# Optimization experiments

Measured on AMD Instinct MI355X. Metric: run time of the kernel, lower is better.

The kernel has to match this reference:

```python
import jax, jax.numpy as jnp
import numpy as np

EPS = 1e-5


def setup_inputs() -> dict:
    key = jax.random.key(0)
    ks = jax.random.split(key, 12)
    B, C, D, H, W = 16, 32, 32, 64, 64
    HID, OUT = 256, 128
    inp = {
        "x": jax.random.normal(ks[0], (B, C, D, H, W), dtype=jnp.float32),
        "bn_gamma": jax.random.normal(ks[1], (C,), dtype=jnp.float32) * 0.1 + 1.0,
        "bn_beta": jax.random.normal(ks[2], (C,), dtype=jnp.float32) * 0.1,
        "w_ih": jax.random.normal(ks[3], (HID, C), dtype=jnp.float32) / np.sqrt(C),
        "b_ih": jax.random.normal(ks[4], (HID,), dtype=jnp.float32) * 0.01,
        "w_hh": jax.random.normal(ks[5], (HID, HID), dtype=jnp.float32) / np.sqrt(HID),
        "b_hh": jax.random.normal(ks[6], (HID,), dtype=jnp.float32) * 0.01,
        "w_out": jax.random.normal(ks[7], (OUT, HID), dtype=jnp.float32) / np.sqrt(HID),
        "b_out": jax.random.normal(ks[8], (OUT,), dtype=jnp.float32) * 0.01,
        "ln_gamma": jnp.ones((OUT,), dtype=jnp.float32),
        "ln_beta": jnp.zeros((OUT,), dtype=jnp.float32),
        "pooled_depth": 8,
    }
    return inp


def reference(x, bn_gamma, bn_beta, w_ih, b_ih, w_hh, b_hh, w_out, b_out, ln_gamma, ln_beta, pooled_depth):
    B, C, D, H, W = x.shape
    P = pooled_depth
    # SyncBatchNorm (training mode: batch statistics over B, D, H, W per channel)
    mean = jnp.mean(x, axis=(0, 2, 3, 4), keepdims=True)
    var = jnp.mean((x - mean) ** 2, axis=(0, 2, 3, 4), keepdims=True)  # biased var
    g = bn_gamma.reshape(1, C, 1, 1, 1)
    b = bn_beta.reshape(1, C, 1, 1, 1)
    x = (x - mean) * jax.lax.rsqrt(var + EPS) * g + b
    x = jax.nn.relu(x)
    # AdaptiveMaxPool3d -> (P, 1, 1); D divisible by P so bins are uniform
    x = x.reshape(B, C, P, D // P, H, W).max(axis=(3, 4, 5))  # (B, C, P)
    x = jnp.transpose(x, (2, 0, 1))  # (P, B, C) -- time-major
    # RNNCell (relu) scan over time
    hx0 = jnp.zeros((B, w_hh.shape[0]), dtype=x.dtype)

    def step(hx, xt):
        hx = jax.nn.relu(xt @ w_ih.T + b_ih + hx @ w_hh.T + b_hh)
        return hx, None

    hx, _ = jax.lax.scan(step, hx0, x)
    # Output projection + LayerNorm
    out = hx @ w_out.T + b_out  # (B, OUT)
    mu = jnp.mean(out, axis=-1, keepdims=True)
    v = jnp.mean((out - mu) ** 2, axis=-1, keepdims=True)
    out = (out - mu) * jax.lax.rsqrt(v + EPS) * ln_gamma + ln_beta
    return out
```

## Files before the change

kernel.cpp:

```cpp
#include <hip/hip_runtime.h>
#include <math.h>
#include <stdint.h>

#define EPS 1e-5f

constexpr int Bc = 16, Cc = 32, Pc = 8, HIDc = 256, OUTc = 128;
constexpr int NBINS = 4096;
constexpr float NPC_INV = 1.0f / 2097152.0f;

constexpr size_t WHH16_BYTE  = 65536;
constexpr size_t WOUT16_BYTE = 196608;

typedef float fx4 __attribute__((ext_vector_type(4)));

__device__ inline uint32_t bf16_rne(float f) {
    uint32_t u = __float_as_uint(f);
    return (u + 0x7fffu + ((u >> 16) & 1u)) >> 16;
}

__global__ __launch_bounds__(256) void k1_stats(const float* __restrict__ x,
                                                float* __restrict__ ws,
                                                const float* __restrict__ w_hh,
                                                const float* __restrict__ w_out) {
    const int bid = blockIdx.x;
    const int t = threadIdx.x;

    if (bid < 192) {
        const bool hh = bid < 128;
        const float* src = hh ? w_hh : w_out;
        uint32_t* dst = (uint32_t*)((char*)ws + (hh ? WHH16_BYTE : WOUT16_BYTE));
        const int i = (hh ? bid : bid - 128) * 512 + t * 2;
        const float a = src[i], b = src[i + 1];
        dst[i >> 1] = bf16_rne(a) | (bf16_rne(b) << 16);
    }

    const fx4* px = reinterpret_cast<const fx4*>(x) + ((size_t)bid << 12);

    float vmax = -INFINITY, vmin = INFINITY, s = 0.f, ss = 0.f;
#pragma unroll
    for (int j = 0; j < 16; ++j) {
        fx4 v = __builtin_nontemporal_load(&px[j * 256 + t]);
        vmax = fmaxf(vmax, fmaxf(fmaxf(v.x, v.y), fmaxf(v.z, v.w)));
        vmin = fminf(vmin, fminf(fminf(v.x, v.y), fminf(v.z, v.w)));
        s += (v.x + v.y) + (v.z + v.w);
        ss = fmaf(v.x, v.x, ss); ss = fmaf(v.y, v.y, ss);
        ss = fmaf(v.z, v.z, ss); ss = fmaf(v.w, v.w, ss);
    }
#pragma unroll
    for (int off = 1; off < 64; off <<= 1) {
        vmax = fmaxf(vmax, __shfl_xor(vmax, off));
        vmin = fminf(vmin, __shfl_xor(vmin, off));
        s += __shfl_xor(s, off);
        ss += __shfl_xor(ss, off);
    }
    __shared__ float r[4][4];
    const int wid = t >> 6;
    if ((t & 63) == 0) { r[wid][0] = vmax; r[wid][1] = vmin; r[wid][2] = s; r[wid][3] = ss; }
    __syncthreads();
    if (t == 0) {
        vmax = fmaxf(fmaxf(r[0][0], r[1][0]), fmaxf(r[2][0], r[3][0]));
        vmin = fminf(fminf(r[0][1], r[1][1]), fminf(r[2][1], r[3][1]));
        s  = (r[0][2] + r[1][2]) + (r[2][2] + r[3][2]);
        ss = (r[0][3] + r[1][3]) + (r[2][3] + r[3][3]);
        ws[bid]             = vmax;
        ws[NBINS + bid]     = vmin;
        ws[2 * NBINS + bid] = s;
        ws[3 * NBINS + bid] = ss;
    }
}

__global__ __launch_bounds__(512, 2) void k2_rnn(const float* __restrict__ ws,
                                                 const float* __restrict__ bn_gamma,
                                                 const float* __restrict__ bn_beta,
                                                 const float* __restrict__ w_ih,
                                                 const float* __restrict__ b_ih,
                                                 const float* __restrict__ b_hh,
                                                 const float* __restrict__ b_out,
                                                 const float* __restrict__ ln_gamma,
                                                 const float* __restrict__ ln_beta,
                                                 float* __restrict__ out) {
    const int b = blockIdx.x;
    const int t = threadIdx.x;
    const int og = t >> 3, kg = t & 7;

    const uint32_t* whh16  = (const uint32_t*)((const char*)ws + WHH16_BYTE);
    const uint32_t* wout16 = (const uint32_t*)((const char*)ws + WOUT16_BYTE);

    __shared__ float scale_s[Cc], shift_s[Cc];
    __shared__ float pA[2][Cc], pB[2][Cc];
    __shared__ __align__(16) float pooled[Pc][Cc];
    __shared__ __align__(16) float u[Pc][HIDc];
    __shared__ __align__(16) float hxs[2][288];
    __shared__ __align__(16) float o[OUTc];
    __shared__ float red2[2];

    {
        const float* sums = ws + 2 * NBINS;
        const float* sqs  = ws + 3 * NBINS;
        float s = 0.f, ss = 0.f;
#pragma unroll
        for (int j = 0; j < 8; ++j) {
            s  += sums[t + 512 * j];
            ss += sqs[t + 512 * j];
        }
#pragma unroll
        for (int off = 1; off < 8; off <<= 1) {
            s  += __shfl_xor(s, off);
            ss += __shfl_xor(ss, off);
        }
        if ((t & 7) == 0) {
            pA[t >> 8][(t >> 3) & 31] = s;
            pB[t >> 8][(t >> 3) & 31] = ss;
        }
    }

    uint32_t wpk[4][16];
#pragma unroll
    for (int r = 0; r < 4; ++r) {
        const uint4* wrow = reinterpret_cast<const uint4*>(whh16 + (4 * og + r) * 128 + 16 * kg);
#pragma unroll
        for (int q = 0; q < 4; ++q) {
            uint4 v = wrow[q];
            wpk[r][4 * q + 0] = v.x; wpk[r][4 * q + 1] = v.y;
            wpk[r][4 * q + 2] = v.z; wpk[r][4 * q + 3] = v.w;
        }
    }

    __syncthreads();

    float4 w4[4][8];
#pragma unroll
    for (int r = 0; r < 4; ++r) {
#pragma unroll
        for (int e = 0; e < 8; ++e) {
            const uint32_t u0 = wpk[r][2 * e], u1 = wpk[r][2 * e + 1];
            w4[r][e].x = __uint_as_float(u0 << 16);
            w4[r][e].y = __uint_as_float(u0 & 0xFFFF0000u);
            w4[r][e].z = __uint_as_float(u1 << 16);
            w4[r][e].w = __uint_as_float(u1 & 0xFFFF0000u);
        }
    }
    if (t < Cc) {
        const float s = pA[0][t] + pA[1][t], ss = pB[0][t] + pB[1][t];
        const float mean = s * NPC_INV;
        const float var  = ss * NPC_INV - mean * mean;
        const float sc   = bn_gamma[t] * rsqrtf(var + EPS);
        scale_s[t] = sc;
        shift_s[t] = bn_beta[t] - mean * sc;
    }
    __syncthreads();

    if (t < 256) {
        const int c = t >> 3;
        const int bin = b * 256 + t;
        const float sc = scale_s[c];
        const float xm = (sc >= 0.f) ? ws[bin] : ws[NBINS + bin];
        pooled[t & 7][c] = fmaxf(fmaf(sc, xm, shift_s[c]), 0.f);
    }
    __syncthreads();

    {
        const int h = t & 255, pg = t >> 8;
        const float4* wi = reinterpret_cast<const float4*>(w_ih) + h * (Cc / 4);
        float4 wiv[8];
#pragma unroll
        for (int e = 0; e < 8; ++e) wiv[e] = wi[e];
        const float bias = b_ih[h] + b_hh[h];
        float u0 = 0.f;
#pragma unroll
        for (int pp = 0; pp < 4; ++pp) {
            const int p = pg * 4 + pp;
            const float4* pl = reinterpret_cast<const float4*>(&pooled[p][0]);
            float a0 = bias, a1 = 0.f, a2 = 0.f, a3 = 0.f;
#pragma unroll
            for (int e = 0; e < 8; ++e) {
                float4 pv = pl[e];
                a0 = fmaf(pv.x, wiv[e].x, a0);
                a1 = fmaf(pv.y, wiv[e].y, a1);
                a2 = fmaf(pv.z, wiv[e].z, a2);
                a3 = fmaf(pv.w, wiv[e].w, a3);
            }
            const float uv = (a0 + a1) + (a2 + a3);
            u[p][h] = uv;
            if (pp == 0) u0 = uv;
        }
        if (pg == 0) hxs[0][36 * (h >> 5) + (h & 31)] = fmaxf(u0, 0.f);
    }
    __syncthreads();

    int cur = 0;
    for (int step = 1; step < Pc; ++step) {
        float4 h4[8];
        const float4* hp = reinterpret_cast<const float4*>(&hxs[cur][kg * 36]);
#pragma unroll
        for (int e = 0; e < 8; ++e) h4[e] = hp[e];
        float acc[4];
#pragma unroll
        for (int r = 0; r < 4; ++r) {
            float a0 = 0.f, a1 = 0.f, a2 = 0.f, a3 = 0.f;
#pragma unroll
            for (int e = 0; e < 8; ++e) {
                float4 wv = w4[r][e], hv = h4[e];
                a0 = fmaf(hv.x, wv.x, a0);
                a1 = fmaf(hv.y, wv.y, a1);
                a2 = fmaf(hv.z, wv.z, a2);
                a3 = fmaf(hv.w, wv.w, a3);
            }
            acc[r] = (a0 + a1) + (a2 + a3);
        }
#pragma unroll
        for (int off = 1; off < 8; off <<= 1) {
#pragma unroll
            for (int r = 0; r < 4; ++r) acc[r] += __shfl_xor(acc[r], off);
        }
        if (kg == 0) {
#pragma unroll
            for (int r = 0; r < 4; ++r) {
                const int h = 4 * og + r;
                const float v = u[step][h] + acc[r];
                hxs[cur ^ 1][36 * (h >> 5) + (h & 31)] = fmaxf(v, 0.f);
            }
        }
        __syncthreads();
        cur ^= 1;
    }

    {
        const int oi = t >> 2, seg = t & 3;
        const uint4* wop = reinterpret_cast<const uint4*>(wout16) + oi * 32 + seg * 8;
        float a0 = ((t & 3) == 0) ? b_out[oi] : 0.f, a1 = 0.f, a2 = 0.f, a3 = 0.f;
#pragma unroll
        for (int e = 0; e < 8; ++e) {
            const uint4 pk = wop[e];
            const int k = seg * 64 + e * 8;
            const int base = 36 * (k >> 5) + (k & 31);
            const float4 hv0 = *reinterpret_cast<const float4*>(&hxs[1][base]);
            const float4 hv1 = *reinterpret_cast<const float4*>(&hxs[1][base + 4]);
            a0 = fmaf(hv0.x, __uint_as_float(pk.x << 16), a0);
            a1 = fmaf(hv0.y, __uint_as_float(pk.x & 0xFFFF0000u), a1);
            a2 = fmaf(hv0.z, __uint_as_float(pk.y << 16), a2);
            a3 = fmaf(hv0.w, __uint_as_float(pk.y & 0xFFFF0000u), a3);
            a0 = fmaf(hv1.x, __uint_as_float(pk.z << 16), a0);
            a1 = fmaf(hv1.y, __uint_as_float(pk.z & 0xFFFF0000u), a1);
            a2 = fmaf(hv1.z, __uint_as_float(pk.w << 16), a2);
            a3 = fmaf(hv1.w, __uint_as_float(pk.w & 0xFFFF0000u), a3);
        }
        float s = (a0 + a1) + (a2 + a3);
        s += __shfl_xor(s, 1);
        s += __shfl_xor(s, 2);
        if (seg == 0) o[oi] = s;
    }
    __syncthreads();

    if (t < 64) {
        const float x0 = o[t], x1 = o[t + 64];
        float s = x0 + x1, ss = x0 * x0 + x1 * x1;
#pragma unroll
        for (int off = 1; off < 64; off <<= 1) {
            s  += __shfl_xor(s, off);
            ss += __shfl_xor(ss, off);
        }
        if (t == 0) { red2[0] = s; red2[1] = ss; }
    }
    __syncthreads();
    if (t < OUTc) {
        const float mu  = red2[0] * (1.0f / OUTc);
        const float var = red2[1] * (1.0f / OUTc) - mu * mu;
        const float rs  = rsqrtf(var + EPS);
        out[b * OUTc + t] = (o[t] - mu) * rs * ln_gamma[t] + ln_beta[t];
    }
}

extern "C" void kernel_launch(void* const* d_in, const int* in_sizes, int n_in,
                              void* d_out, int out_size, void* d_ws, size_t ws_size,
                              hipStream_t stream) {
    const float* x        = (const float*)d_in[0];
    const float* bn_gamma = (const float*)d_in[1];
    const float* bn_beta  = (const float*)d_in[2];
    const float* w_ih     = (const float*)d_in[3];
    const float* b_ih     = (const float*)d_in[4];
    const float* w_hh     = (const float*)d_in[5];
    const float* b_hh     = (const float*)d_in[6];
    const float* w_out    = (const float*)d_in[7];
    const float* b_out    = (const float*)d_in[8];
    const float* ln_gamma = (const float*)d_in[9];
    const float* ln_beta  = (const float*)d_in[10];
    float* out = (float*)d_out;
    float* ws  = (float*)d_ws;

    k1_stats<<<NBINS, 256, 0, stream>>>(x, ws, w_hh, w_out);
    k2_rnn<<<Bc, 512, 0, stream>>>(ws, bn_gamma, bn_beta, w_ih, b_ih, b_hh,
                                   b_out, ln_gamma, ln_beta, out);
}
```

Baseline: 60.90 us.

## Widen RNN kernel to 1024 threads and prefetch all weights up front

The recurrent kernel now runs 1024 threads per batch block, with 4 threads per hidden unit instead of 8 threads covering 4 units each. This shortens the per-step dot product and the shuffle reduction on the serial recurrence. All global loads (recurrent weights, output weights, pooled bins, biases, layernorm params) are issued at kernel start so their latency overlaps the statistics reduction. The costs are more threads per block, added register pressure from the preloaded output weights, and a tighter launch-bounds occupancy target.

```diff
diff --git a/kernel.cpp b/kernel.cpp
--- a/kernel.cpp
+++ b/kernel.cpp
@@ -69,39 +69,60 @@
     }
 }
 
-__global__ __launch_bounds__(512, 2) void k2_rnn(const float* __restrict__ ws,
-                                                 const float* __restrict__ bn_gamma,
-                                                 const float* __restrict__ bn_beta,
-                                                 const float* __restrict__ w_ih,
-                                                 const float* __restrict__ b_ih,
-                                                 const float* __restrict__ b_hh,
-                                                 const float* __restrict__ b_out,
-                                                 const float* __restrict__ ln_gamma,
-                                                 const float* __restrict__ ln_beta,
-                                                 float* __restrict__ out) {
+__global__ __launch_bounds__(1024, 4) void k2_rnn(const float* __restrict__ ws,
+                                                  const float* __restrict__ bn_gamma,
+                                                  const float* __restrict__ bn_beta,
+                                                  const float* __restrict__ w_ih,
+                                                  const float* __restrict__ b_ih,
+                                                  const float* __restrict__ b_hh,
+                                                  const float* __restrict__ b_out,
+                                                  const float* __restrict__ ln_gamma,
+                                                  const float* __restrict__ ln_beta,
+                                                  float* __restrict__ out) {
     const int b = blockIdx.x;
     const int t = threadIdx.x;
-    const int og = t >> 3, kg = t & 7;
+    const int h = t >> 2, q = t & 3;
+    const int oi = t >> 3, seg = t & 7;
 
     const uint32_t* whh16  = (const uint32_t*)((const char*)ws + WHH16_BYTE);
     const uint32_t* wout16 = (const uint32_t*)((const char*)ws + WOUT16_BYTE);
 
     __shared__ float scale_s[Cc], shift_s[Cc];
-    __shared__ float pA[2][Cc], pB[2][Cc];
+    __shared__ float pA[4][Cc], pB[4][Cc];
     __shared__ __align__(16) float pooled[Pc][Cc];
     __shared__ __align__(16) float u[Pc][HIDc];
     __shared__ __align__(16) float hxs[2][288];
     __shared__ __align__(16) float o[OUTc];
     __shared__ float red2[2];
 
+    uint4 wpk4[8];
+    {
+        const uint4* wr = reinterpret_cast<const uint4*>(whh16 + h * 128 + q * 32);
+#pragma unroll
+        for (int e = 0; e < 8; ++e) wpk4[e] = wr[e];
+    }
+    uint4 wopk[4];
+    {
+        const uint4* wr = reinterpret_cast<const uint4*>(wout16 + oi * 128 + seg * 16);
+#pragma unroll
+        for (int e = 0; e < 4; ++e) wopk[e] = wr[e];
+    }
+    float xmaxv = 0.f, xminv = 0.f;
+    if (t < 256) { xmaxv = ws[b * 256 + t]; xminv = ws[NBINS + b * 256 + t]; }
+    const int h_c = t & 255;
+    const float bias_c = b_ih[h_c] + b_hh[h_c];
+    const float bout_e = (seg == 0) ? b_out[oi] : 0.f;
+    float lng = 0.f, lnb = 0.f;
+    if (t < OUTc) { lng = ln_gamma[t]; lnb = ln_beta[t]; }
+
     {
         const float* sums = ws + 2 * NBINS;
         const float* sqs  = ws + 3 * NBINS;
         float s = 0.f, ss = 0.f;
 #pragma unroll
-        for (int j = 0; j < 8; ++j) {
-            s  += sums[t + 512 * j];
-            ss += sqs[t + 512 * j];
+        for (int j = 0; j < 4; ++j) {
+            s  += sums[t + 1024 * j];
+            ss += sqs[t + 1024 * j];
         }
 #pragma unroll
         for (int off = 1; off < 8; off <<= 1) {
@@ -113,35 +134,24 @@
             pB[t >> 8][(t >> 3) & 31] = ss;
         }
     }
-
-    uint32_t wpk[4][16];
-#pragma unroll
-    for (int r = 0; r < 4; ++r) {
-        const uint4* wrow = reinterpret_cast<const uint4*>(whh16 + (4 * og + r) * 128 + 16 * kg);
-#pragma unroll
-        for (int q = 0; q < 4; ++q) {
-            uint4 v = wrow[q];
-            wpk[r][4 * q + 0] = v.x; wpk[r][4 * q + 1] = v.y;
-            wpk[r][4 * q + 2] = v.z; wpk[r][4 * q + 3] = v.w;
-        }
-    }
-
-    __syncthreads();
-
-    float4 w4[4][8];
-#pragma unroll
-    for (int r = 0; r < 4; ++r) {
-#pragma unroll
-        for (int e = 0; e < 8; ++e) {
-            const uint32_t u0 = wpk[r][2 * e], u1 = wpk[r][2 * e + 1];
-            w4[r][e].x = __uint_as_float(u0 << 16);
-            w4[r][e].y = __uint_as_float(u0 & 0xFFFF0000u);
-            w4[r][e].z = __uint_as_float(u1 << 16);
-            w4[r][e].w = __uint_as_float(u1 & 0xFFFF0000u);
-        }
+    __syncthreads();
+
+    float4 w4[16];
+#pragma unroll
+    for (int e = 0; e < 8; ++e) {
+        const uint4 pk = wpk4[e];
+        w4[2 * e].x     = __uint_as_float(pk.x << 16);
+        w4[2 * e].y     = __uint_as_float(pk.x & 0xFFFF0000u);
+        w4[2 * e].z     = __uint_as_float(pk.y << 16);
+        w4[2 * e].w     = __uint_as_float(pk.y & 0xFFFF0000u);
+        w4[2 * e + 1].x = __uint_as_float(pk.z << 16);
+        w4[2 * e + 1].y = __uint_as_float(pk.z & 0xFFFF0000u);
+        w4[2 * e + 1].z = __uint_as_float(pk.w << 16);
+        w4[2 * e + 1].w = __uint_as_float(pk.w & 0xFFFF0000u);
     }
     if (t < Cc) {
-        const float s = pA[0][t] + pA[1][t], ss = pB[0][t] + pB[1][t];
+        const float s  = pA[0][t] + pA[1][t] + pA[2][t] + pA[3][t];
+        const float ss = pB[0][t] + pB[1][t] + pB[2][t] + pB[3][t];
         const float mean = s * NPC_INV;
         const float var  = ss * NPC_INV - mean * mean;
         const float sc   = bn_gamma[t] * rsqrtf(var + EPS);
@@ -152,26 +162,24 @@
 
     if (t < 256) {
         const int c = t >> 3;
-        const int bin = b * 256 + t;
         const float sc = scale_s[c];
-        const float xm = (sc >= 0.f) ? ws[bin] : ws[NBINS + bin];
+        const float xm = (sc >= 0.f) ? xmaxv : xminv;
         pooled[t & 7][c] = fmaxf(fmaf(sc, xm, shift_s[c]), 0.f);
     }
     __syncthreads();
 
     {
-        const int h = t & 255, pg = t >> 8;
-        const float4* wi = reinterpret_cast<const float4*>(w_ih) + h * (Cc / 4);
+        const int pg = t >> 8;
+        const float4* wi = reinterpret_cast<const float4*>(w_ih) + h_c * (Cc / 4);
         float4 wiv[8];
 #pragma unroll
         for (int e = 0; e < 8; ++e) wiv[e] = wi[e];
-        const float bias = b_ih[h] + b_hh[h];
         float u0 = 0.f;
 #pragma unroll
-        for (int pp = 0; pp < 4; ++pp) {
-            const int p = pg * 4 + pp;
+        for (int pp = 0; pp < 2; ++pp) {
+            const int p = pg * 2 + pp;
             const float4* pl = reinterpret_cast<const float4*>(&pooled[p][0]);
-            float a0 = bias, a1 = 0.f, a2 = 0.f, a3 = 0.f;
+            float a0 = bias_c, a1 = 0.f, a2 = 0.f, a3 = 0.f;
 #pragma unroll
             for (int e = 0; e < 8; ++e) {
                 float4 pv = pl[e];
@@ -181,59 +189,51 @@
                 a3 = fmaf(pv.w, wiv[e].w, a3);
             }
             const float uv = (a0 + a1) + (a2 + a3);
-            u[p][h] = uv;
+            u[p][h_c] = uv;
             if (pp == 0) u0 = uv;
         }
-        if (pg == 0) hxs[0][36 * (h >> 5) + (h & 31)] = fmaxf(u0, 0.f);
+        if (pg == 0) hxs[0][36 * (h_c >> 5) + (h_c & 31)] = fmaxf(u0, 0.f);
     }
     __syncthreads();
 
     int cur = 0;
     for (int step = 1; step < Pc; ++step) {
-        float4 h4[8];
-        const float4* hp = reinterpret_cast<const float4*>(&hxs[cur][kg * 36]);
-#pragma unroll
-        for (int e = 0; e < 8; ++e) h4[e] = hp[e];
-        float acc[4];
-#pragma unroll
-        for (int r = 0; r < 4; ++r) {
-            float a0 = 0.f, a1 = 0.f, a2 = 0.f, a3 = 0.f;
-#pragma unroll
-            for (int e = 0; e < 8; ++e) {
-                float4 wv = w4[r][e], hv = h4[e];
-                a0 = fmaf(hv.x, wv.x, a0);
-                a1 = fmaf(hv.y, wv.y, a1);
-                a2 = fmaf(hv.z, wv.z, a2);
-                a3 = fmaf(hv.w, wv.w, a3);
+        const float* hbase = &hxs[cur][72 * q];
+        float a0 = 0.f, a1 = 0.f, a2 = 0.f, a3 = 0.f;
+#pragma unroll
+        for (int c4 = 0; c4 < 4; ++c4) {
+            float4 hv[4];
+#pragma unroll
+            for (int e = 0; e < 4; ++e) {
+                const int ee = c4 * 4 + e;
+                hv[e] = *reinterpret_cast<const float4*>(hbase + 36 * (ee >> 3) + 4 * (ee & 7));
             }
-            acc[r] = (a0 + a1) + (a2 + a3);
-        }
-#pragma unroll
-        for (int off = 1; off < 8; off <<= 1) {
-#pragma unroll
-            for (int r = 0; r < 4; ++r) acc[r] += __shfl_xor(acc[r], off);
-        }
-        if (kg == 0) {
-#pragma unroll
-            for (int r = 0; r < 4; ++r) {
-                const int h = 4 * og + r;
-                const float v = u[step][h] + acc[r];
-                hxs[cur ^ 1][36 * (h >> 5) + (h & 31)] = fmaxf(v, 0.f);
+#pragma unroll
+            for (int e = 0; e < 4; ++e) {
+                const float4 wv = w4[c4 * 4 + e];
+                a0 = fmaf(hv[e].x, wv.x, a0);
+                a1 = fmaf(hv[e].y, wv.y, a1);
+                a2 = fmaf(hv[e].z, wv.z, a2);
+                a3 = fmaf(hv[e].w, wv.w, a3);
             }
+        }
+        float acc = (a0 + a1) + (a2 + a3);
+        acc += __shfl_xor(acc, 1);
+        acc += __shfl_xor(acc, 2);
+        if (q == 0) {
+            const float v = u[step][h] + acc;
+            hxs[cur ^ 1][36 * (h >> 5) + (h & 31)] = fmaxf(v, 0.f);
         }
         __syncthreads();
         cur ^= 1;
     }
 
     {
-        const int oi = t >> 2, seg = t & 3;
-        const uint4* wop = reinterpret_cast<const uint4*>(wout16) + oi * 32 + seg * 8;
-        float a0 = ((t & 3) == 0) ? b_out[oi] : 0.f, a1 = 0.f, a2 = 0.f, a3 = 0.f;
-#pragma unroll
-        for (int e = 0; e < 8; ++e) {
-            const uint4 pk = wop[e];
-            const int k = seg * 64 + e * 8;
-            const int base = 36 * (k >> 5) + (k & 31);
+        float a0 = bout_e, a1 = 0.f, a2 = 0.f, a3 = 0.f;
+#pragma unroll
+        for (int e = 0; e < 4; ++e) {
+            const uint4 pk = wopk[e];
+            const int base = 36 * seg + 8 * e;
             const float4 hv0 = *reinterpret_cast<const float4*>(&hxs[1][base]);
             const float4 hv1 = *reinterpret_cast<const float4*>(&hxs[1][base + 4]);
             a0 = fmaf(hv0.x, __uint_as_float(pk.x << 16), a0);
@@ -248,6 +248,7 @@
         float s = (a0 + a1) + (a2 + a3);
         s += __shfl_xor(s, 1);
         s += __shfl_xor(s, 2);
+        s += __shfl_xor(s, 4);
         if (seg == 0) o[oi] = s;
     }
     __syncthreads();
@@ -267,7 +268,7 @@
         const float mu  = red2[0] * (1.0f / OUTc);
         const float var = red2[1] * (1.0f / OUTc) - mu * mu;
         const float rs  = rsqrtf(var + EPS);
-        out[b * OUTc + t] = (o[t] - mu) * rs * ln_gamma[t] + ln_beta[t];
+        out[b * OUTc + t] = (o[t] - mu) * rs * lng + lnb;
     }
 }
 
@@ -289,6 +290,6 @@
     float* ws  = (float*)d_ws;
 
     k1_stats<<<NBINS, 256, 0, stream>>>(x, ws, w_hh, w_out);
-    k2_rnn<<<Bc, 512, 0, stream>>>(ws, bn_gamma, bn_beta, w_ih, b_ih, b_hh,
-                                   b_out, ln_gamma, ln_beta, out);
-}
+    k2_rnn<<<Bc, 1024, 0, stream>>>(ws, bn_gamma, bn_beta, w_ih, b_ih, b_hh,
+                                    b_out, ln_gamma, ln_beta, out);
+}
```

Measured after the change: 62.02 us. No clear change (+1.8%).
